# Kernel tuning notes

Hardware: AMD Instinct MI355X
Metric: run time of the kernel (lower is better)

Reference implementation:

```python
import jax, jax.numpy as jnp
import numpy as np

B = 16384
S0, S1 = 7, 7
NB, NC = 2, 20
WC, WN = 5.0, 0.5  # weight_coord, weight_noobject
D = NB * 5 + NC  # 30


def setup_inputs() -> dict:
    key = jax.random.key(0)
    k1, k2, k3, k4 = jax.random.split(key, 4)
    predication = jax.random.normal(k1, (B, S0 * S1 * D), dtype=jnp.float32)
    grid = jax.random.randint(k2, (B, S0, S1), 0, 2, dtype=jnp.int32)
    tbox = jax.random.uniform(k3, (B, S0, S1, 4), dtype=jnp.float32)
    # keep target w,h strictly positive (real boxes), offsets in [0,1)
    tbox = tbox.at[..., 2:].set(0.05 + 0.9 * tbox[..., 2:])
    tcls = jax.random.randint(k4, (B, S0, S1), 0, NC, dtype=jnp.int32)
    return {"predication": predication, "grid": grid, "tbox": tbox, "tcls": tcls}


def _yolo_loss(predication, grid, tbox, tcls):
    pred = predication.reshape(B, S0, S1, D)
    conf = jax.nn.sigmoid(pred[..., :NB])                                  # (B,S0,S1,NB)
    pb = jax.nn.sigmoid(pred[..., NB:5 * NB]).reshape(B, S0, S1, NB, 4)    # (B,S0,S1,NB,4)
    cls = jax.nn.softmax(pred[..., 5 * NB:], axis=-1)                      # (B,S0,S1,NC)

    # cell coordinates: x = column index, y = row index (matches the [1,0] swap in torch code)
    xg = jnp.arange(S1, dtype=pred.dtype)[None, None, :]   # (1,1,S1)
    yg = jnp.arange(S0, dtype=pred.dtype)[None, :, None]   # (1,S0,1)

    tox, toy, tw, th = tbox[..., 0], tbox[..., 1], tbox[..., 2], tbox[..., 3]
    tcx = (xg + tox) / S0
    tcy = (yg + toy) / S1

    pcx = (xg[..., None] + pb[..., 0]) / S0   # (B,S0,S1,NB)
    pcy = (yg[..., None] + pb[..., 1]) / S1
    pw, ph = pb[..., 2], pb[..., 3]

    # IOU of each predicted box vs the cell's target box (same formula as _calc_iou)
    tb_ = jnp.minimum(tcx[..., None] + tw[..., None] / 2, pcx + pw / 2) - \
          jnp.maximum(tcx[..., None] - tw[..., None] / 2, pcx - pw / 2)
    lr_ = jnp.minimum(tcy[..., None] + th[..., None] / 2, pcy + ph / 2) - \
          jnp.maximum(tcy[..., None] - th[..., None] / 2, pcy - ph / 2)
    inter = jnp.where((tb_ < 0) | (lr_ < 0), 0.0, tb_ * lr_)
    iou = inter / ((tw * th)[..., None] + pw * ph - inter)                 # (B,S0,S1,NB)

    # best predictor chosen on detached IOUs (original uses pred_boxes.detach())
    best = jnp.argmax(jax.lax.stop_gradient(iou), axis=-1)                 # (B,S0,S1)

    take = lambda a: jnp.take_along_axis(a, best[..., None], axis=-1)[..., 0]
    iou_b = take(iou)          # attached IOU re-used in confidence loss
    conf_b = take(conf)
    pbb = jnp.take_along_axis(pb, best[..., None, None], axis=3)[..., 0, :]  # (B,S0,S1,4)

    cls_t = jnp.take_along_axis(cls, tcls[..., None], axis=-1)[..., 0]

    coord = (pbb[..., 0] - tox) ** 2 + (pbb[..., 1] - toy) ** 2 \
          + (jnp.sqrt(pbb[..., 2]) - jnp.sqrt(tw)) ** 2 \
          + (jnp.sqrt(pbb[..., 3]) - jnp.sqrt(th)) ** 2

    obj_loss = WC * coord + (conf_b - iou_b) ** 2 + (1.0 - cls_t) ** 2     # (B,S0,S1)
    noobj_loss = WN * jnp.sum(conf ** 2, axis=-1)                          # (B,S0,S1)

    objm = (grid == 1).astype(pred.dtype)
    total = jnp.sum(objm * obj_loss + (1.0 - objm) * noobj_loss)
    return total / B


def reference(predication, grid, tbox, tcls):
    return _yolo_loss(predication, grid, tbox, tcls)
```

## Files before the change

kernel.cpp:

```cpp
#include <hip/hip_runtime.h>
#include <math.h>

namespace {

constexpr int kB    = 16384;
constexpr int kS0   = 7;
constexpr int kS1   = 7;
constexpr int kD    = 30;
constexpr int kCells = kB * kS0 * kS1;
constexpr int TPB   = 256;
constexpr int NBLK  = kCells / TPB;
constexpr int NSLOT = 64;
constexpr float kInv7 = 1.0f / 7.0f;
constexpr float kWC = 5.0f;
constexpr float kWN = 0.5f;

__device__ __forceinline__ float sigm(float x) {
    return 1.0f / (1.0f + __expf(-x));
}

__global__ void __launch_bounds__(TPB, 4) yolo_loss_kernel(
    const float* __restrict__ pred,
    const int*   __restrict__ grid,
    const float* __restrict__ tbox,
    const int*   __restrict__ tcls,
    float* __restrict__ partials)
{
    __shared__ float sp[TPB * kD];
    __shared__ float wsum[TPB / 64];

    const int tid   = threadIdx.x;
    const int cell0 = blockIdx.x * TPB;
    const int cell  = cell0 + tid;
    const int wave  = tid >> 6;
    const int lane  = tid & 63;

    const float4* __restrict__ g4 =
        reinterpret_cast<const float4*>(pred + (size_t)cell0 * kD);
    float4* s4 = reinterpret_cast<float4*>(sp);
    const int etid = 1792 + (tid & 127);

    float4 r[8];
    #pragma unroll
    for (int k = 0; k < 7; ++k) r[k] = g4[tid + 256 * k];
    r[7] = g4[etid];

    const float4 tb4 = reinterpret_cast<const float4*>(tbox)[cell];
    const int g  = grid[cell];
    const int tc = tcls[cell];

    __builtin_amdgcn_sched_barrier(0);

    #pragma unroll
    for (int k = 0; k < 7; ++k) s4[tid + 256 * k] = r[k];
    s4[etid] = r[7];
    __syncthreads();

    const int cj = cell % kS1;
    const int ci = (cell / kS1) % kS0;

    float f[kD];
    {
        const float2* p2 = reinterpret_cast<const float2*>(sp + tid * kD);
        #pragma unroll
        for (int q = 0; q < kD / 2; ++q) {
            float2 t = p2[q];
            f[2 * q]     = t.x;
            f[2 * q + 1] = t.y;
        }
    }

    const float tox = tb4.x, toy = tb4.y, tw = tb4.z, th = tb4.w;

    const float conf0 = sigm(f[0]);
    const float conf1 = sigm(f[1]);
    float pbx[2], pby[2], pbw[2], pbh[2];
    #pragma unroll
    for (int k = 0; k < 2; ++k) {
        pbx[k] = sigm(f[2 + 4 * k + 0]);
        pby[k] = sigm(f[2 + 4 * k + 1]);
        pbw[k] = sigm(f[2 + 4 * k + 2]);
        pbh[k] = sigm(f[2 + 4 * k + 3]);
    }

    float cmax = f[10];
    #pragma unroll
    for (int q = 11; q < 30; ++q) cmax = fmaxf(cmax, f[q]);
    float csum = 0.0f, et = 0.0f;
    #pragma unroll
    for (int q = 0; q < 20; ++q) {
        const float e = __expf(f[10 + q] - cmax);
        csum += e;
        et = (q == tc) ? e : et;
    }
    const float cls_t = et / csum;

    const float x = (float)cj, y = (float)ci;
    const float tcx = (x + tox) * kInv7;
    const float tcy = (y + toy) * kInv7;
    const float thw = tw * 0.5f, thh = th * 0.5f;
    const float tarea = tw * th;

    float iou[2];
    #pragma unroll
    for (int k = 0; k < 2; ++k) {
        const float pcx = (x + pbx[k]) * kInv7;
        const float pcy = (y + pby[k]) * kInv7;
        const float pw = pbw[k], ph = pbh[k];
        const float tb_ = fminf(tcx + thw, pcx + pw * 0.5f) - fmaxf(tcx - thw, pcx - pw * 0.5f);
        const float lr_ = fminf(tcy + thh, pcy + ph * 0.5f) - fmaxf(tcy - thh, pcy - ph * 0.5f);
        float inter = tb_ * lr_;
        inter = (tb_ < 0.0f || lr_ < 0.0f) ? 0.0f : inter;
        iou[k] = inter / (tarea + pw * ph - inter);
    }

    const bool b1 = (iou[1] > iou[0]);
    const float bx = b1 ? pbx[1] : pbx[0];
    const float by = b1 ? pby[1] : pby[0];
    const float bw = b1 ? pbw[1] : pbw[0];
    const float bh = b1 ? pbh[1] : pbh[0];
    const float conf_b = b1 ? conf1 : conf0;
    const float iou_b  = b1 ? iou[1] : iou[0];

    const float dx = bx - tox;
    const float dy = by - toy;
    const float dw = sqrtf(bw) - sqrtf(tw);
    const float dh = sqrtf(bh) - sqrtf(th);
    const float coord = dx * dx + dy * dy + dw * dw + dh * dh;
    const float d1 = conf_b - iou_b;
    const float d2 = 1.0f - cls_t;
    const float obj   = kWC * coord + d1 * d1 + d2 * d2;
    const float noobj = kWN * (conf0 * conf0 + conf1 * conf1);

    float v = (g == 1) ? obj : noobj;

    #pragma unroll
    for (int off = 32; off > 0; off >>= 1) v += __shfl_down(v, off, 64);
    if (lane == 0) wsum[wave] = v;
    __syncthreads();
    if (tid == 0) {
        atomicAdd(&partials[blockIdx.x & (NSLOT - 1)],
                  wsum[0] + wsum[1] + wsum[2] + wsum[3]);
    }
}

__global__ void finish_kernel(const float* __restrict__ partials,
                              float* __restrict__ out)
{
    float v = partials[threadIdx.x];
    #pragma unroll
    for (int off = 32; off > 0; off >>= 1) v += __shfl_down(v, off, 64);
    if (threadIdx.x == 0) out[0] = v * (1.0f / kB);
}

}

extern "C" void kernel_launch(void* const* d_in, const int* in_sizes, int n_in,
                              void* d_out, int out_size, void* d_ws, size_t ws_size,
                              hipStream_t stream) {
    const float* pred = (const float*)d_in[0];
    const int*   grid = (const int*)d_in[1];
    const float* tbox = (const float*)d_in[2];
    const int*   tcls = (const int*)d_in[3];
    float* out      = (float*)d_out;
    float* partials = (float*)d_ws;

    hipMemsetAsync(partials, 0, NSLOT * sizeof(float), stream);
    yolo_loss_kernel<<<NBLK, TPB, 0, stream>>>(pred, grid, tbox, tcls, partials);
    finish_kernel<<<1, 64, 0, stream>>>(partials, out);
}
```

Measured before the change: 160.4 us.

## Process four tiles per block with register prefetch; drop softmax max and use rcp

Each block now handles four 256-cell tiles. It prefetches the next tile's predictions and targets into registers while computing the current tile, then stages them through shared memory between barriers. The softmax no longer subtracts the max before exponentiation, and divisions are replaced by the hardware reciprocal approximation. This aims to overlap global loads with compute and cut ALU work. In exchange it adds register pressure and extra barriers, and it risks overflow or precision loss for large logits.

Result: slower. 187.8 us (+17.1%).

```diff
diff --git a/kernel.cpp b/kernel.cpp
--- a/kernel.cpp
+++ b/kernel.cpp
@@ -9,14 +9,97 @@
 constexpr int kD    = 30;
 constexpr int kCells = kB * kS0 * kS1;
 constexpr int TPB   = 256;
-constexpr int NBLK  = kCells / TPB;
+constexpr int T     = 4;
+constexpr int NBLK  = kCells / (TPB * T);
 constexpr int NSLOT = 64;
 constexpr float kInv7 = 1.0f / 7.0f;
 constexpr float kWC = 5.0f;
 constexpr float kWN = 0.5f;
 
+__device__ __forceinline__ float frcp(float x) {
+    return __builtin_amdgcn_rcpf(x);
+}
+
 __device__ __forceinline__ float sigm(float x) {
-    return 1.0f / (1.0f + __expf(-x));
+    return frcp(1.0f + __expf(-x));
+}
+
+__device__ __forceinline__ float cell_loss(const float* __restrict__ sp, int tid,
+                                           int cell, float4 tb4, int g, int tc)
+{
+    float f[kD];
+    {
+        const float2* p2 = reinterpret_cast<const float2*>(sp + tid * kD);
+        #pragma unroll
+        for (int q = 0; q < kD / 2; ++q) {
+            float2 t = p2[q];
+            f[2 * q]     = t.x;
+            f[2 * q + 1] = t.y;
+        }
+    }
+
+    const int cj = cell % kS1;
+    const int ci = (cell / kS1) % kS0;
+    const float tox = tb4.x, toy = tb4.y, tw = tb4.z, th = tb4.w;
+
+    const float conf0 = sigm(f[0]);
+    const float conf1 = sigm(f[1]);
+    float pbx[2], pby[2], pbw[2], pbh[2];
+    #pragma unroll
+    for (int k = 0; k < 2; ++k) {
+        pbx[k] = sigm(f[2 + 4 * k + 0]);
+        pby[k] = sigm(f[2 + 4 * k + 1]);
+        pbw[k] = sigm(f[2 + 4 * k + 2]);
+        pbh[k] = sigm(f[2 + 4 * k + 3]);
+    }
+
+    float csum = 0.0f, et = 0.0f;
+    #pragma unroll
+    for (int q = 0; q < 20; ++q) {
+        const float e = __expf(f[10 + q]);
+        csum += e;
+        et = (q == tc) ? e : et;
+    }
+    const float cls_t = et * frcp(csum);
+
+    const float x = (float)cj, y = (float)ci;
+    const float tcx = (x + tox) * kInv7;
+    const float tcy = (y + toy) * kInv7;
+    const float thw = tw * 0.5f, thh = th * 0.5f;
+    const float tarea = tw * th;
+
+    float iou[2];
+    #pragma unroll
+    for (int k = 0; k < 2; ++k) {
+        const float pcx = (x + pbx[k]) * kInv7;
+        const float pcy = (y + pby[k]) * kInv7;
+        const float pw = pbw[k], ph = pbh[k];
+        const float tb_ = fminf(tcx + thw, pcx + pw * 0.5f) - fmaxf(tcx - thw, pcx - pw * 0.5f);
+        const float lr_ = fminf(tcy + thh, pcy + ph * 0.5f) - fmaxf(tcy - thh, pcy - ph * 0.5f);
+        float inter = tb_ * lr_;
+        inter = (tb_ < 0.0f || lr_ < 0.0f) ? 0.0f : inter;
+        iou[k] = inter * frcp(tarea + pw * ph - inter);
+    }
+
+    const bool b1 = (iou[1] > iou[0]);
+    const float bx = b1 ? pbx[1] : pbx[0];
+    const float by = b1 ? pby[1] : pby[0];
+    const float bw = b1 ? pbw[1] : pbw[0];
+    const float bh = b1 ? pbh[1] : pbh[0];
+    const float conf_b = b1 ? conf1 : conf0;
+    const float iou_b  = b1 ? iou[1] : iou[0];
+
+    const float dx = bx - tox;
+    const float dy = by - toy;
+    const float dw = sqrtf(bw) - sqrtf(tw);
+    const float dh = sqrtf(bh) - sqrtf(th);
+    const float coord = dx * dx + dy * dy + dw * dw + dh * dh;
+    const float d1 = conf_b - iou_b;
+    const float d2 = 1.0f - cls_t;
+    const float obj   = kWC * coord + d1 * d1 + d2 * d2;
+    const float noobj = kWN * (conf0 * conf0 + conf1 * conf1);
+
+    return (g == 1) ? obj : noobj;
 }
 
 __global__ void __launch_bounds__(TPB, 4) yolo_loss_kernel(
@@ -30,109 +113,57 @@
     __shared__ float wsum[TPB / 64];
 
     const int tid   = threadIdx.x;
-    const int cell0 = blockIdx.x * TPB;
-    const int cell  = cell0 + tid;
     const int wave  = tid >> 6;
     const int lane  = tid & 63;
-
-    const float4* __restrict__ g4 =
-        reinterpret_cast<const float4*>(pred + (size_t)cell0 * kD);
+    const int tile0 = blockIdx.x * T;
+    const int etid  = 1792 + (tid & 127);
+
     float4* s4 = reinterpret_cast<float4*>(sp);
-    const int etid = 1792 + (tid & 127);
-
-    float4 r[8];
-    #pragma unroll
-    for (int k = 0; k < 7; ++k) r[k] = g4[tid + 256 * k];
-    r[7] = g4[etid];
-
-    const float4 tb4 = reinterpret_cast<const float4*>(tbox)[cell];
-    const int g  = grid[cell];
-    const int tc = tcls[cell];
-
-    __builtin_amdgcn_sched_barrier(0);
-
+    const float4* __restrict__ tb4p = reinterpret_cast<const float4*>(tbox);
+
+    float4 r[8]; float4 tb; int gg, tc;
+    {
+        const float4* g4 = reinterpret_cast<const float4*>(
+            pred + (size_t)tile0 * TPB * kD);
+        #pragma unroll
+        for (int k = 0; k < 7; ++k) r[k] = g4[tid + 256 * k];
+        r[7] = g4[etid];
+        const int c = tile0 * TPB + tid;
+        tb = tb4p[c]; gg = grid[c]; tc = tcls[c];
+        __builtin_amdgcn_sched_barrier(0);
+    }
     #pragma unroll
     for (int k = 0; k < 7; ++k) s4[tid + 256 * k] = r[k];
     s4[etid] = r[7];
     __syncthreads();
 
-    const int cj = cell % kS1;
-    const int ci = (cell / kS1) % kS0;
-
-    float f[kD];
-    {
-        const float2* p2 = reinterpret_cast<const float2*>(sp + tid * kD);
-        #pragma unroll
-        for (int q = 0; q < kD / 2; ++q) {
-            float2 t = p2[q];
-            f[2 * q]     = t.x;
-            f[2 * q + 1] = t.y;
+    float v = 0.0f;
+    #pragma unroll
+    for (int t = 0; t < T; ++t) {
+        const int cell = (tile0 + t) * TPB + tid;
+
+        float4 rn[8]; float4 tbn; int gn, tcn;
+        if (t + 1 < T) {
+            const float4* g4n = reinterpret_cast<const float4*>(
+                pred + (size_t)(tile0 + t + 1) * TPB * kD);
+            #pragma unroll
+            for (int k = 0; k < 7; ++k) rn[k] = g4n[tid + 256 * k];
+            rn[7] = g4n[etid];
+            tbn = tb4p[cell + TPB]; gn = grid[cell + TPB]; tcn = tcls[cell + TPB];
+            __builtin_amdgcn_sched_barrier(0);
         }
-    }
-
-    const float tox = tb4.x, toy = tb4.y, tw = tb4.z, th = tb4.w;
-
-    const float conf0 = sigm(f[0]);
-    const float conf1 = sigm(f[1]);
-    float pbx[2], pby[2], pbw[2], pbh[2];
-    #pragma unroll
-    for (int k = 0; k < 2; ++k) {
-        pbx[k] = sigm(f[2 + 4 * k + 0]);
-        pby[k] = sigm(f[2 + 4 * k + 1]);
-        pbw[k] = sigm(f[2 + 4 * k + 2]);
-        pbh[k] = sigm(f[2 + 4 * k + 3]);
-    }
-
-    float cmax = f[10];
-    #pragma unroll
-    for (int q = 11; q < 30; ++q) cmax = fmaxf(cmax, f[q]);
-    float csum = 0.0f, et = 0.0f;
-    #pragma unroll
-    for (int q = 0; q < 20; ++q) {
-        const float e = __expf(f[10 + q] - cmax);
-        csum += e;
-        et = (q == tc) ? e : et;
-    }
-    const float cls_t = et / csum;
-
-    const float x = (float)cj, y = (float)ci;
-    const float tcx = (x + tox) * kInv7;
-    const float tcy = (y + toy) * kInv7;
-    const float thw = tw * 0.5f, thh = th * 0.5f;
-    const float tarea = tw * th;
-
-    float iou[2];
-    #pragma unroll
-    for (int k = 0; k < 2; ++k) {
-        const float pcx = (x + pbx[k]) * kInv7;
-        const float pcy = (y + pby[k]) * kInv7;
-        const float pw = pbw[k], ph = pbh[k];
-        const float tb_ = fminf(tcx + thw, pcx + pw * 0.5f) - fmaxf(tcx - thw, pcx - pw * 0.5f);
-        const float lr_ = fminf(tcy + thh, pcy + ph * 0.5f) - fmaxf(tcy - thh, pcy - ph * 0.5f);
-        float inter = tb_ * lr_;
-        inter = (tb_ < 0.0f || lr_ < 0.0f) ? 0.0f : inter;
-        iou[k] = inter / (tarea + pw * ph - inter);
-    }
-
-    const bool b1 = (iou[1] > iou[0]);
-    const float bx = b1 ? pbx[1] : pbx[0];
-    const float by = b1 ? pby[1] : pby[0];
-    const float bw = b1 ? pbw[1] : pbw[0];
-    const float bh = b1 ? pbh[1] : pbh[0];
-    const float conf_b = b1 ? conf1 : conf0;
-    const float iou_b  = b1 ? iou[1] : iou[0];
-
-    const float dx = bx - tox;
-    const float dy = by - toy;
-    const float dw = sqrtf(bw) - sqrtf(tw);
-    const float dh = sqrtf(bh) - sqrtf(th);
-    const float coord = dx * dx + dy * dy + dw * dw + dh * dh;
-    const float d1 = conf_b - iou_b;
-    const float d2 = 1.0f - cls_t;
-    const float obj   = kWC * coord + d1 * d1 + d2 * d2;
-    const float noobj = kWN * (conf0 * conf0 + conf1 * conf1);
-
-    float v = (g == 1) ? obj : noobj;
+
+        v += cell_loss(sp, tid, cell, tb, gg, tc);
+
+        if (t + 1 < T) {
+            __syncthreads();
+            #pragma unroll
+            for (int k = 0; k < 7; ++k) s4[tid + 256 * k] = rn[k];
+            s4[etid] = rn[7];
+            __syncthreads();
+            tb = tbn; gg = gn; tc = tcn;
+        }
+    }
 
     #pragma unroll
     for (int off = 32; off > 0; off >>= 1) v += __shfl_down(v, off, 64);
```
